# Kernel optimization log

Measured on AMD Instinct MI355X. Metric: run time of the kernel, lower is better.

## Reference

```python
import jax, jax.numpy as jnp
import numpy as np

B, T, NH, EX, VOCAB, NLAYER = 8, 510, 12, 768, 256, 6
NBLK = 2 * NLAYER - 1          # 11 blocks, all with out=ex
NE = T + 2                     # CustomEmb output dim = n_embd = 512
HD = EX // NH
EXIT_SCALE = 1.0 / float(np.sqrt(4 * NBLK))  # torch init divides 'exit' params by sqrt(#exit params)


def _ln(x, s, b):
    m = jnp.mean(x, axis=-1, keepdims=True)
    v = jnp.mean((x - m) ** 2, axis=-1, keepdims=True)
    return (x - m) * jax.lax.rsqrt(v + 1e-5) * s + b


def setup_inputs() -> dict:
    key = jax.random.key(0)
    ks = iter(jax.random.split(key, 40))
    def n(shape, scale=0.02):
        return jax.random.normal(next(ks), shape, jnp.float32) * scale
    inp = {}
    inp['idx'] = jax.random.randint(next(ks), (B, T), 0, 2)
    inp['lin_w'] = n((NE, EX)); inp['lin_b'] = n((EX,))
    # stacked per-block params (leading dim NBLK), torch Linear math y = x @ W + b with W stored (in,out)
    inp['ln1_s'] = jnp.ones((NBLK, EX), jnp.float32); inp['ln1_b'] = jnp.zeros((NBLK, EX), jnp.float32)
    inp['qw'] = n((NBLK, EX, EX)); inp['qb'] = n((NBLK, EX))
    inp['kw'] = n((NBLK, EX, EX)); inp['kb'] = n((NBLK, EX))
    inp['vw'] = n((NBLK, EX, EX)); inp['vb'] = n((NBLK, EX))
    inp['ew'] = n((NBLK, EX, EX)) * EXIT_SCALE; inp['eb'] = n((NBLK, EX)) * EXIT_SCALE
    inp['ln2_s'] = jnp.ones((NBLK, EX), jnp.float32); inp['ln2_b'] = jnp.zeros((NBLK, EX), jnp.float32)
    inp['m1w'] = n((NBLK, EX, 4 * EX)); inp['m1b'] = n((NBLK, 4 * EX))
    inp['m2w'] = n((NBLK, 4 * EX, EX)) * EXIT_SCALE; inp['m2b'] = n((NBLK, EX)) * EXIT_SCALE
    inp['lnf_s'] = jnp.ones((EX,), jnp.float32); inp['lnf_b'] = jnp.zeros((EX,), jnp.float32)
    inp['head_w'] = n((EX * T, VOCAB)); inp['head_b'] = n((VOCAB,))
    return inp


def reference(idx, lin_w, lin_b, ln1_s, ln1_b, qw, qb, kw, kb, vw, vb, ew, eb,
              ln2_s, ln2_b, m1w, m1b, m2w, m2b, lnf_s, lnf_b, head_w, head_b):
    # CustomEmb: one-hot of binary token + identity positional encoding -> [B,T,T+2]
    e0 = (idx == 0).astype(jnp.float32)
    e1 = (idx == 1).astype(jnp.float32)
    pos = jnp.broadcast_to(jnp.eye(T, dtype=jnp.float32), (B, T, T))
    x = jnp.concatenate([e0[:, :, None], e1[:, :, None], pos], axis=2)
    x = jax.nn.relu(x @ lin_w + lin_b)                       # [B,T,EX]
    mask = jnp.tril(jnp.ones((T, T), bool))
    inv_sqrt_d = 1.0 / float(np.sqrt(HD))

    def block(x, p):
        l1s, l1b, Qw, Qb, Kw, Kb, Vw, Vb, Ew, Eb, l2s, l2b, M1w, M1b, M2w, M2b = p
        h = _ln(x, l1s, l1b)
        q = (h @ Qw + Qb).reshape(B, T, NH, HD)
        k = (h @ Kw + Kb).reshape(B, T, NH, HD)
        v = (h @ Vw + Vb).reshape(B, T, NH, HD)
        att = jnp.einsum('bqhd,bkhd->bhqk', q, k) * inv_sqrt_d
        att = jnp.where(mask, att, -jnp.inf)
        probs = jax.nn.softmax(att, axis=-1)
        y = jnp.einsum('bhqk,bkhd->bqhd', probs, v).reshape(B, T, EX)
        x = x + y @ Ew + Eb
        h2 = _ln(x, l2s, l2b)
        x = x + jax.nn.relu(h2 @ M1w + M1b) @ M2w + M2b      # MLP depth=2: initial+relu+exit
        return x, None

    x, _ = jax.lax.scan(block, x, (ln1_s, ln1_b, qw, qb, kw, kb, vw, vb,
                                   ew, eb, ln2_s, ln2_b, m1w, m1b, m2w, m2b))
    x = _ln(x, lnf_s, lnf_b)
    return x.reshape(B, -1) @ head_w + head_b                # [B, VOCAB]
```

## Files before the change

### kernel.cpp

```cpp
#include <hip/hip_runtime.h>
#include <hip/hip_bf16.h>
#include <math.h>

constexpr int cB = 8, cT = 510, cNH = 12, cEX = 768, cVOC = 256, cNBLK = 11, cHD = 64;
constexpr int cMB = 512;
constexpr int cMP = 4096;
constexpr int cQKV = 3 * cEX;

typedef __attribute__((ext_vector_type(8))) short bf16x8;
typedef __attribute__((ext_vector_type(4))) float f32x4;
using bf16 = __hip_bfloat16;

__device__ inline void gload16(const void* g, void* l) {
    __builtin_amdgcn_global_load_lds((const __attribute__((address_space(1))) unsigned int*)g,
                                     (__attribute__((address_space(3))) unsigned int*)l, 16, 0, 0);
}
__device__ inline short f2bs(float f) {
    bf16 b = __float2bfloat16(f);
    return *reinterpret_cast<short*>(&b);
}
__device__ inline float bs2f(unsigned short s) {
    unsigned int u = ((unsigned int)s) << 16;
    float f;
    __builtin_memcpy(&f, &u, 4);
    return f;
}

__global__ __launch_bounds__(256) void embed_kernel(
    const int* __restrict__ idx, const float* __restrict__ lin_w,
    const float* __restrict__ lin_b, short* __restrict__ x)
{
    int row = blockIdx.x;
    int b = row >> 9, t = row & 511;
    short* xr = x + (size_t)row * cEX;
    if (t >= cT) {
        for (int j = threadIdx.x; j < cEX; j += 256) xr[j] = 0;
        return;
    }
    int tok = idx[b * cT + t] & 1;
    const float* wt = lin_w + (size_t)tok * cEX;
    const float* wp = lin_w + (size_t)(2 + t) * cEX;
    for (int j = threadIdx.x; j < cEX; j += 256) {
        float val = wt[j] + wp[j] + lin_b[j];
        xr[j] = f2bs(fmaxf(val, 0.0f));
    }
}

__global__ __launch_bounds__(256) void ln_wave(
    const short* __restrict__ in, const float* __restrict__ s,
    const float* __restrict__ bsh, short* __restrict__ out)
{
    const int wid = threadIdx.x >> 6, lane = threadIdx.x & 63;
    const int row = blockIdx.x * 4 + wid;
    const short* xr = in + (size_t)row * cEX;
    float v[12];
    float sum = 0.f, sq = 0.f;
#pragma unroll
    for (int p = 0; p < 3; ++p) {
        ushort4 raw = *(const ushort4*)&xr[p * 256 + lane * 4];
        v[p * 4 + 0] = bs2f(raw.x); v[p * 4 + 1] = bs2f(raw.y);
        v[p * 4 + 2] = bs2f(raw.z); v[p * 4 + 3] = bs2f(raw.w);
#pragma unroll
        for (int q = 0; q < 4; ++q) { sum += v[p * 4 + q]; sq += v[p * 4 + q] * v[p * 4 + q]; }
    }
#pragma unroll
    for (int off = 1; off < 64; off <<= 1) {
        sum += __shfl_xor(sum, off, 64);
        sq  += __shfl_xor(sq, off, 64);
    }
    float mean = sum * (1.0f / cEX);
    float var = sq * (1.0f / cEX) - mean * mean;
    float rstd = rsqrtf(var + 1e-5f);
    short* outr = out + (size_t)row * cEX;
#pragma unroll
    for (int p = 0; p < 3; ++p) {
        int c = p * 256 + lane * 4;
        float4 sv = *(const float4*)&s[c];
        float4 bv = *(const float4*)&bsh[c];
        short4 pk;
        pk.x = f2bs((v[p * 4 + 0] - mean) * rstd * sv.x + bv.x);
        pk.y = f2bs((v[p * 4 + 1] - mean) * rstd * sv.y + bv.y);
        pk.z = f2bs((v[p * 4 + 2] - mean) * rstd * sv.z + bv.z);
        pk.w = f2bs((v[p * 4 + 3] - mean) * rstd * sv.w + bv.w);
        *(short4*)&outr[c] = pk;
    }
}

__global__ __launch_bounds__(256) void transpose_w(
    const float* __restrict__ W, bf16* __restrict__ WT,
    int K, int N, size_t w_stride, size_t wt_stride, int wt_row_off)
{
    __shared__ float t[32][33];
    const float* Wb = W + (size_t)blockIdx.z * w_stride;
    bf16* WTb = WT + (size_t)blockIdx.z * wt_stride;
    int n0 = blockIdx.x * 32, k0 = blockIdx.y * 32;
    int c = threadIdx.x & 31, ty = threadIdx.x >> 5;
#pragma unroll
    for (int it = 0; it < 4; ++it) {
        int r = ty + it * 8;
        t[r][c] = Wb[(size_t)(k0 + r) * N + n0 + c];
    }
    __syncthreads();
#pragma unroll
    for (int it = 0; it < 4; ++it) {
        int a = ty + it * 8;
        WTb[(size_t)(wt_row_off + n0 + a) * K + k0 + c] = __float2bfloat16(t[c][a]);
    }
}

__global__ __launch_bounds__(256) void transpose_qkv(
    const float* __restrict__ qw, const float* __restrict__ kw,
    const float* __restrict__ vw, bf16* __restrict__ WT)
{
    __shared__ float t[32][33];
    int z = blockIdx.z;
    int blk = z / 3, which = z - blk * 3;
    const float* Wb = (which == 0 ? qw : which == 1 ? kw : vw) + (size_t)blk * cEX * cEX;
    bf16* WTb = WT + (size_t)blk * cQKV * cEX + (size_t)which * cEX * cEX;
    int n0 = blockIdx.x * 32, k0 = blockIdx.y * 32;
    int c = threadIdx.x & 31, ty = threadIdx.x >> 5;
#pragma unroll
    for (int it = 0; it < 4; ++it) {
        int r = ty + it * 8;
        t[r][c] = Wb[(size_t)(k0 + r) * cEX + n0 + c];
    }
    __syncthreads();
#pragma unroll
    for (int it = 0; it < 4; ++it) {
        int a = ty + it * 8;
        WTb[(size_t)(n0 + a) * cEX + k0 + c] = __float2bfloat16(t[c][a]);
    }
}

__global__ __launch_bounds__(256) void concat_bias(
    const float* __restrict__ qb, const float* __restrict__ kb,
    const float* __restrict__ vb, float* __restrict__ qkvb)
{
    int i = blockIdx.x * 256 + threadIdx.x;
    if (i >= cNBLK * cQKV) return;
    int blk = i / cQKV, c = i - blk * cQKV;
    const float* src; int cc = c;
    if (c < cEX)            { src = qb; }
    else if (c < 2 * cEX)   { src = kb; cc = c - cEX; }
    else                    { src = vb; cc = c - 2 * cEX; }
    qkvb[i] = src[(size_t)blk * cEX + cc];
}

template<int FM, int FN, bool RELU, bool RESID, bool OUTBF16, bool VT>
__global__ __launch_bounds__(256) void gemm_db(
    const short* __restrict__ A, const short* __restrict__ BT,
    const float* __restrict__ bias, const short* __restrict__ resid,
    void* __restrict__ Cout, short* __restrict__ vTr, int K, int N)
{
    constexpr int BM = FM * 32, BN = FN * 32;
    constexpr int TS = (BM + BN) * 64;
    constexpr int CA = BM / 32, CB = BN / 32;
    constexpr int LPT = CA + CB;
    static_assert(LPT >= 5 && LPT <= 8, "vmcnt literal range");
    __shared__ short lds[2 * TS];
    const int tid = threadIdx.x;
    const int lane = tid & 63, wid = tid >> 6;
    const int wm = wid >> 1, wn = wid & 1;
    const int bm = blockIdx.y * BM, bn = blockIdx.x * BN;
    const int li = lane & 15, gk = lane >> 4;

    f32x4 acc[FM][FN];
#pragma unroll
    for (int i = 0; i < FM; ++i)
#pragma unroll
        for (int j = 0; j < FN; ++j)
            acc[i][j] = f32x4{0.f, 0.f, 0.f, 0.f};

    auto stage = [&](int kt, int buf) {
        short* la = &lds[buf * TS];
        short* lb = la + BM * 64;
#pragma unroll
        for (int i = 0; i < CA; ++i) {
            int s = i * 256 + tid;
            int r = s >> 3, c = s & 7;
            gload16(A + (size_t)(bm + r) * K + kt * 64 + (c ^ (r & 7)) * 8,
                    (char*)la + (size_t)(i * 256 + wid * 64) * 16);
        }
#pragma unroll
        for (int i = 0; i < CB; ++i) {
            int s = i * 256 + tid;
            int r = s >> 3, c = s & 7;
            gload16(BT + (size_t)(bn + r) * K + kt * 64 + (c ^ (r & 7)) * 8,
                    (char*)lb + (size_t)(i * 256 + wid * 64) * 16);
        }
    };

    const int nkt = K >> 6;
    stage(0, 0);
    stage(1, 1);

    for (int t = 0; t < nkt; ++t) {
        if (t + 1 < nkt) {
            if constexpr (LPT == 5)      asm volatile("s_waitcnt vmcnt(5)" ::: "memory");
            else if constexpr (LPT == 6) asm volatile("s_waitcnt vmcnt(6)" ::: "memory");
            else if constexpr (LPT == 7) asm volatile("s_waitcnt vmcnt(7)" ::: "memory");
            else                         asm volatile("s_waitcnt vmcnt(8)" ::: "memory");
        } else {
            asm volatile("s_waitcnt vmcnt(0)" ::: "memory");
        }
        __builtin_amdgcn_s_barrier();

        const short* la = &lds[(t & 1) * TS];
        const short* lb = la + BM * 64;

        bf16x8 af0[FM], bf0[FN];
#pragma unroll
        for (int mi = 0; mi < FM; ++mi) {
            int row = (wm * FM + mi) * 16 + li;
            af0[mi] = *(const bf16x8*)&la[row * 64 + (gk ^ (row & 7)) * 8];
        }
#pragma unroll
        for (int ni = 0; ni < FN; ++ni) {
            int row = (wn * FN + ni) * 16 + li;
            bf0[ni] = *(const bf16x8*)&lb[row * 64 + (gk ^ (row & 7)) * 8];
        }
        __builtin_amdgcn_s_setprio(1);
#pragma unroll
        for (int mi = 0; mi < FM; ++mi)
#pragma unroll
            for (int ni = 0; ni < FN; ++ni)
                acc[mi][ni] = __builtin_amdgcn_mfma_f32_16x16x32_bf16(
                    af0[mi], bf0[ni], acc[mi][ni], 0, 0, 0);
        __builtin_amdgcn_s_setprio(0);

        bf16x8 af1[FM], bf1[FN];
#pragma unroll
        for (int mi = 0; mi < FM; ++mi) {
            int row = (wm * FM + mi) * 16 + li;
            af1[mi] = *(const bf16x8*)&la[row * 64 + ((4 + gk) ^ (row & 7)) * 8];
        }
#pragma unroll
        for (int ni = 0; ni < FN; ++ni) {
            int row = (wn * FN + ni) * 16 + li;
            bf1[ni] = *(const bf16x8*)&lb[row * 64 + ((4 + gk) ^ (row & 7)) * 8];
        }
        asm volatile("s_waitcnt lgkmcnt(0)" ::: "memory");
        __builtin_amdgcn_s_barrier();
        if (t + 2 < nkt) stage(t + 2, t & 1);
        __builtin_amdgcn_s_setprio(1);
#pragma unroll
        for (int mi = 0; mi < FM; ++mi)
#pragma unroll
            for (int ni = 0; ni < FN; ++ni)
                acc[mi][ni] = __builtin_amdgcn_mfma_f32_16x16x32_bf16(
                    af1[mi], bf1[ni], acc[mi][ni], 0, 0, 0);
        __builtin_amdgcn_s_setprio(0);
    }

#pragma unroll
    for (int mi = 0; mi < FM; ++mi) {
#pragma unroll
        for (int ni = 0; ni < FN; ++ni) {
            int col = bn + (wn * FN + ni) * 16 + li;
            float bv = bias[col];
            int row0 = bm + (wm * FM + mi) * 16 + gk * 4;
            if (VT && col >= 2 * cEX) {
                short4 pk;
                pk.x = f2bs(acc[mi][ni][0] + bv);
                pk.y = f2bs(acc[mi][ni][1] + bv);
                pk.z = f2bs(acc[mi][ni][2] + bv);
                pk.w = f2bs(acc[mi][ni][3] + bv);
                *(short4*)&vTr[(size_t)(col - 2 * cEX) * cMP + row0] = pk;
            } else {
#pragma unroll
                for (int j = 0; j < 4; ++j) {
                    int row = row0 + j;
                    float v = acc[mi][ni][j] + bv;
                    if (RELU) v = fmaxf(v, 0.0f);
                    if (RESID) v += bs2f((unsigned short)resid[(size_t)row * N + col]);
                    if (OUTBF16)
                        ((bf16*)Cout)[(size_t)row * N + col] = __float2bfloat16(v);
                    else
                        ((float*)Cout)[(size_t)row * N + col] = v;
                }
            }
        }
    }
}

__global__ __launch_bounds__(256) void attn_mfma(
    const short* __restrict__ qkv, const short* __restrict__ vT, bf16* __restrict__ y)
{
    const int qt = blockIdx.x, h = blockIdx.y, b = blockIdx.z;
    __shared__ short Ks[2][64 * 64];
    __shared__ short Vs[2][64 * 64];
    __shared__ short Ss[4][16][72];
    const int tid = threadIdx.x;
    const int lane = tid & 63, wid = tid >> 6;
    const int li = lane & 15, gk = lane >> 4;

    const size_t rowb = (size_t)b * cMB;
    int qr = qt * 64 + wid * 16 + li;
    int qrc = qr < cT ? qr : cT - 1;
    const short* qrow = qkv + (rowb + qrc) * cQKV + h * cHD;
    bf16x8 qf0 = *(const bf16x8*)(qrow + gk * 8);
    bf16x8 qf1 = *(const bf16x8*)(qrow + 32 + gk * 8);

    f32x4 o[4];
    float mrow[4], lrow[4];
#pragma unroll
    for (int dt = 0; dt < 4; ++dt) o[dt] = f32x4{0.f, 0.f, 0.f, 0.f};
#pragma unroll
    for (int j = 0; j < 4; ++j) { mrow[j] = -3e38f; lrow[j] = 0.f; }

    const int qloc = qt * 64 + wid * 16 + gk * 4;

    auto stage = [&](int kt, int buf) {
#pragma unroll
        for (int i = 0; i < 2; ++i) {
            int s = i * 256 + tid;
            int r = s >> 3, c = s & 7;
            gload16(qkv + (rowb + kt * 64 + r) * cQKV + cEX + h * cHD + (c ^ (r & 7)) * 8,
                    (char*)&Ks[buf][0] + (size_t)(i * 256 + wid * 64) * 16);
        }
#pragma unroll
        for (int i = 0; i < 2; ++i) {
            int s = i * 256 + tid;
            int d = s >> 3, c = s & 7;
            gload16(vT + (size_t)(h * cHD + d) * cMP + rowb + kt * 64 + (c ^ (d & 7)) * 8,
                    (char*)&Vs[buf][0] + (size_t)(i * 256 + wid * 64) * 16);
        }
    };

    const int nkt = qt + 1;
    stage(0, 0);
    for (int kt = 0; kt < nkt; ++kt) {
        if (kt + 1 < nkt) {
            stage(kt + 1, (kt + 1) & 1);
            asm volatile("s_waitcnt vmcnt(4)" ::: "memory");
        } else {
            asm volatile("s_waitcnt vmcnt(0)" ::: "memory");
        }
        __builtin_amdgcn_s_barrier();
        const int cur = kt & 1;

        f32x4 sg[4];
#pragma unroll
        for (int g = 0; g < 4; ++g) sg[g] = f32x4{0.f, 0.f, 0.f, 0.f};
#pragma unroll
        for (int g = 0; g < 4; ++g) {
            int key = g * 16 + li;
            bf16x8 k0 = *(const bf16x8*)&Ks[cur][key * 64 + (gk ^ (key & 7)) * 8];
            bf16x8 k1 = *(const bf16x8*)&Ks[cur][key * 64 + ((4 + gk) ^ (key & 7)) * 8];
            sg[g] = __builtin_amdgcn_mfma_f32_16x16x32_bf16(qf0, k0, sg[g], 0, 0, 0);
            sg[g] = __builtin_amdgcn_mfma_f32_16x16x32_bf16(qf1, k1, sg[g], 0, 0, 0);
        }

#pragma unroll
        for (int j = 0; j < 4; ++j) {
            int q = qloc + j;
            float sc[4];
#pragma unroll
            for (int g = 0; g < 4; ++g) {
                int kg = kt * 64 + g * 16 + li;
                sc[g] = (kg <= q) ? sg[g][j] * 0.125f : -3e38f;
            }
            float tm = fmaxf(fmaxf(sc[0], sc[1]), fmaxf(sc[2], sc[3]));
            tm = fmaxf(tm, __shfl_xor(tm, 1, 16));
            tm = fmaxf(tm, __shfl_xor(tm, 2, 16));
            tm = fmaxf(tm, __shfl_xor(tm, 4, 16));
            tm = fmaxf(tm, __shfl_xor(tm, 8, 16));
            float mnew = fmaxf(mrow[j], tm);
            float p[4], ps = 0.f;
#pragma unroll
            for (int g = 0; g < 4; ++g) { p[g] = __expf(sc[g] - mnew); ps += p[g]; }
            ps += __shfl_xor(ps, 1, 16);
            ps += __shfl_xor(ps, 2, 16);
            ps += __shfl_xor(ps, 4, 16);
            ps += __shfl_xor(ps, 8, 16);
            float scale = __expf(mrow[j] - mnew);
            lrow[j] = lrow[j] * scale + ps;
            mrow[j] = mnew;
#pragma unroll
            for (int dt = 0; dt < 4; ++dt) o[dt][j] *= scale;
#pragma unroll
            for (int g = 0; g < 4; ++g)
                Ss[wid][gk * 4 + j][g * 16 + li] = f2bs(p[g]);
        }

        bf16x8 pa0 = *(const bf16x8*)&Ss[wid][li][gk * 8];
        bf16x8 pa1 = *(const bf16x8*)&Ss[wid][li][32 + gk * 8];
#pragma unroll
        for (int dt = 0; dt < 4; ++dt) {
            int d = dt * 16 + li;
            bf16x8 vf0 = *(const bf16x8*)&Vs[cur][d * 64 + (gk ^ (d & 7)) * 8];
            bf16x8 vf1 = *(const bf16x8*)&Vs[cur][d * 64 + ((4 + gk) ^ (d & 7)) * 8];
            o[dt] = __builtin_amdgcn_mfma_f32_16x16x32_bf16(pa0, vf0, o[dt], 0, 0, 0);
            o[dt] = __builtin_amdgcn_mfma_f32_16x16x32_bf16(pa1, vf1, o[dt], 0, 0, 0);
        }
        asm volatile("s_waitcnt lgkmcnt(0)" ::: "memory");
        __builtin_amdgcn_s_barrier();
    }

#pragma unroll
    for (int j = 0; j < 4; ++j) {
        int q = qloc + j;
        if (q >= cT) continue;
        float inv = 1.0f / lrow[j];
        bf16* yr = y + (rowb + q) * cEX + h * cHD;
#pragma unroll
        for (int dt = 0; dt < 4; ++dt)
            yr[dt * 16 + li] = __float2bfloat16(o[dt][j] * inv);
    }
}

__global__ __launch_bounds__(256) void head_part_kernel(
    const short* __restrict__ x, const float* __restrict__ lnf_s,
    const float* __restrict__ lnf_b, const float* __restrict__ hw,
    float* __restrict__ part)
{
    __shared__ float xs[8][1536];
    __shared__ float stat[16][2];
    const int tid = threadIdx.x;
    const int trow0 = blockIdx.x * 2;
    const int wid = tid >> 6, lane = tid & 63;
    {
        const int g = lane >> 4, li = lane & 15;
        const int p = wid * 4 + g, bb = p >> 1, rr = p & 1;
        const short* xr = x + ((size_t)(bb * cMB + trow0 + rr)) * cEX;
        float sum = 0.f, sq = 0.f;
#pragma unroll
        for (int it = 0; it < 12; ++it) {
            ushort4 raw = *(const ushort4*)&xr[it * 64 + li * 4];
            float a0 = bs2f(raw.x), a1 = bs2f(raw.y), a2 = bs2f(raw.z), a3 = bs2f(raw.w);
            sum += a0 + a1 + a2 + a3;
            sq  += a0 * a0 + a1 * a1 + a2 * a2 + a3 * a3;
        }
#pragma unroll
        for (int off = 8; off > 0; off >>= 1) {
            sum += __shfl_xor(sum, off, 16);
            sq  += __shfl_xor(sq, off, 16);
        }
        if (li == 0) {
            float mean = sum * (1.0f / cEX);
            float var = sq * (1.0f / cEX) - mean * mean;
            stat[p][0] = mean;
            stat[p][1] = rsqrtf(var + 1e-5f);
        }
    }
    __syncthreads();
    for (int i = tid; i < 8 * 1536; i += 256) {
        int bb = i / 1536, kk = i - bb * 1536;
        int rr = kk >= cEX ? 1 : 0;
        int e = kk - rr * cEX;
        float mean = stat[bb * 2 + rr][0], rstd = stat[bb * 2 + rr][1];
        float val = bs2f((unsigned short)x[((size_t)(bb * cMB + trow0 + rr)) * cEX + e]);
        xs[bb][kk] = (val - mean) * rstd * lnf_s[e] + lnf_b[e];
    }
    __syncthreads();
    float acc[8] = {};
    const int k0 = blockIdx.x * 1536;
    const float* wp = hw + (size_t)k0 * cVOC + tid;
    for (int kk = 0; kk < 1536; ++kk) {
        float w = wp[(size_t)kk * cVOC];
#pragma unroll
        for (int bb = 0; bb < 8; ++bb) acc[bb] += xs[bb][kk] * w;
    }
#pragma unroll
    for (int bb = 0; bb < 8; ++bb)
        part[((size_t)blockIdx.x * 8 + bb) * cVOC + tid] = acc[bb];
}

__global__ __launch_bounds__(256) void head_reduce_kernel(
    const float* __restrict__ part, const float* __restrict__ hb, float* __restrict__ out)
{
    int i = blockIdx.x * 256 + threadIdx.x;
    int bb = i >> 8, vv = i & 255;
    float acc = hb[vv];
    for (int c = 0; c < 255; ++c) acc += part[((size_t)c * 8 + bb) * 256 + vv];
    out[i] = acc;
}

extern "C" void kernel_launch(void* const* d_in, const int* in_sizes, int n_in,
                              void* d_out, int out_size, void* d_ws, size_t ws_size,
                              hipStream_t stream) {
    (void)in_sizes; (void)n_in; (void)out_size; (void)ws_size;
    const int*   idx    = (const int*)d_in[0];
    const float* lin_w  = (const float*)d_in[1];
    const float* lin_b  = (const float*)d_in[2];
    const float* ln1_s  = (const float*)d_in[3];
    const float* ln1_b  = (const float*)d_in[4];
    const float* qw     = (const float*)d_in[5];
    const float* qbias  = (const float*)d_in[6];
    const float* kw     = (const float*)d_in[7];
    const float* kbias  = (const float*)d_in[8];
    const float* vw     = (const float*)d_in[9];
    const float* vbias  = (const float*)d_in[10];
    const float* ew     = (const float*)d_in[11];
    const float* ebias  = (const float*)d_in[12];
    const float* ln2_s  = (const float*)d_in[13];
    const float* ln2_b  = (const float*)d_in[14];
    const float* m1w    = (const float*)d_in[15];
    const float* m1b    = (const float*)d_in[16];
    const float* m2w    = (const float*)d_in[17];
    const float* m2b    = (const float*)d_in[18];
    const float* lnf_s  = (const float*)d_in[19];
    const float* lnf_b  = (const float*)d_in[20];
    const float* head_w = (const float*)d_in[21];
    const float* head_b = (const float*)d_in[22];
    float* out = (float*)d_out;

    const size_t act = (size_t)cMP * cEX;
    float* part = (float*)d_ws;
    float* qkvb = part + 255 * 8 * 256;
    short* x    = (short*)(qkvb + cNBLK * cQKV);
    short* qkv  = x + act;
    short* vTr  = qkv + (size_t)cMP * cQKV;
    short* h    = vTr + (size_t)cEX * cMP;
    short* h2   = h + act;
    short* y    = h2 + act;
    short* u    = y + act;
    short* wqkvT = u + (size_t)cMP * 4 * cEX;
    short* weT   = wqkvT + (size_t)cNBLK * cQKV * cEX;
    short* wm1T  = weT + (size_t)cNBLK * cEX * cEX;
    short* wm2T  = wm1T + (size_t)cNBLK * cEX * 4 * cEX;

    transpose_qkv<<<dim3(24, 24, 3 * cNBLK), 256, 0, stream>>>(qw, kw, vw, (bf16*)wqkvT);
    transpose_w<<<dim3(24, 24, cNBLK), 256, 0, stream>>>(ew, (bf16*)weT, cEX, cEX,
        (size_t)cEX * cEX, (size_t)cEX * cEX, 0);
    transpose_w<<<dim3(96, 24, cNBLK), 256, 0, stream>>>(m1w, (bf16*)wm1T, cEX, 4 * cEX,
        (size_t)cEX * 4 * cEX, (size_t)cEX * 4 * cEX, 0);
    transpose_w<<<dim3(24, 96, cNBLK), 256, 0, stream>>>(m2w, (bf16*)wm2T, 4 * cEX, cEX,
        (size_t)cEX * 4 * cEX, (size_t)cEX * 4 * cEX, 0);
    concat_bias<<<(cNBLK * cQKV + 255) / 256, 256, 0, stream>>>(qbias, kbias, vbias, qkvb);

    embed_kernel<<<cMP, 256, 0, stream>>>(idx, lin_w, lin_b, x);

    for (int blk = 0; blk < cNBLK; ++blk) {
        size_t bo = (size_t)blk * cEX;
        ln_wave<<<cMP / 4, 256, 0, stream>>>(x, ln1_s + bo, ln1_b + bo, h);
        gemm_db<4, 3, false, false, true, true><<<dim3(cQKV / 96, cMP / 128), 256, 0, stream>>>(
            h, wqkvT + (size_t)blk * cQKV * cEX, qkvb + (size_t)blk * cQKV, nullptr,
            qkv, vTr, cEX, cQKV);
        attn_mfma<<<dim3(8, cNH, cB), 256, 0, stream>>>(qkv, vTr, (bf16*)y);
        gemm_db<2, 3, false, true, true, false><<<dim3(cEX / 96, cMP / 64), 256, 0, stream>>>(
            y, weT + (size_t)blk * cEX * cEX, ebias + bo, x, x, nullptr, cEX, cEX);
        ln_wave<<<cMP / 4, 256, 0, stream>>>(x, ln2_s + bo, ln2_b + bo, h2);
        gemm_db<4, 4, true, false, true, false><<<dim3(4 * cEX / 128, cMP / 128), 256, 0, stream>>>(
            h2, wm1T + (size_t)blk * cEX * 4 * cEX, m1b + (size_t)blk * 4 * cEX, nullptr,
            u, nullptr, cEX, 4 * cEX);
        gemm_db<2, 3, false, true, true, false><<<dim3(cEX / 96, cMP / 64), 256, 0, stream>>>(
            u, wm2T + (size_t)blk * cEX * 4 * cEX, m2b + bo, x, x, nullptr, 4 * cEX, cEX);
    }
    head_part_kernel<<<255, 256, 0, stream>>>(x, lnf_s, lnf_b, head_w, part);
    head_reduce_kernel<<<8, 256, 0, stream>>>(part, head_b, out);
}
```

Before: 1.718 ms.

## Use 32x32x16 MFMA GEMM with 128x128 tiles for QKV and MLP-up projections

Adds a new GEMM kernel built on 32x32x16 bf16 MFMA instructions with 128x128 block tiles, double-buffered LDS and an XOR-swizzled layout. The QKV projection (which also writes V transposed) and the first MLP projection now use it. The larger MFMA shape cuts LDS fragment loads per FLOP and raises arithmetic intensity. In exchange, the QKV grid changes from 96-wide to 128-wide tiles, and the epilogue stores are strided scalar bf16 writes, which may coalesce poorly.

```diff
diff --git a/kernel.cpp b/kernel.cpp
--- a/kernel.cpp
+++ b/kernel.cpp
@@ -9,6 +9,7 @@
 
 typedef __attribute__((ext_vector_type(8))) short bf16x8;
 typedef __attribute__((ext_vector_type(4))) float f32x4;
+typedef __attribute__((ext_vector_type(16))) float f32x16;
 using bf16 = __hip_bfloat16;
 
 __device__ inline void gload16(const void* g, void* l) {
@@ -146,11 +147,154 @@
     qkvb[i] = src[(size_t)blk * cEX + cc];
 }
 
-template<int FM, int FN, bool RELU, bool RESID, bool OUTBF16, bool VT>
+template<bool RELU, bool VT>
+__global__ __launch_bounds__(256) void gemm32(
+    const short* __restrict__ A, const short* __restrict__ BT,
+    const float* __restrict__ bias, void* __restrict__ Cout,
+    short* __restrict__ vTr, int K, int N)
+{
+    constexpr int BM = 128, BN = 128;
+    constexpr int TS = (BM + BN) * 64;
+    __shared__ short lds[2 * TS];
+    const int tid = threadIdx.x;
+    const int lane = tid & 63, wid = tid >> 6;
+    const int wm = wid >> 1, wn = wid & 1;
+    const int bm = blockIdx.y * BM, bn = blockIdx.x * BN;
+    const int l32 = lane & 31, kh = lane >> 5;
+
+    f32x16 acc[2][2];
+#pragma unroll
+    for (int i = 0; i < 2; ++i)
+#pragma unroll
+        for (int j = 0; j < 2; ++j)
+            acc[i][j] = f32x16{0.f,0.f,0.f,0.f,0.f,0.f,0.f,0.f,
+                               0.f,0.f,0.f,0.f,0.f,0.f,0.f,0.f};
+
+    auto stage = [&](int kt, int buf) {
+        short* la = &lds[buf * TS];
+        short* lb = la + BM * 64;
+#pragma unroll
+        for (int i = 0; i < 4; ++i) {
+            int s = i * 256 + tid;
+            int r = s >> 3, c = s & 7;
+            gload16(A + (size_t)(bm + r) * K + kt * 64 + (c ^ (r & 7)) * 8,
+                    (char*)la + (size_t)(i * 256 + wid * 64) * 16);
+        }
+#pragma unroll
+        for (int i = 0; i < 4; ++i) {
+            int s = i * 256 + tid;
+            int r = s >> 3, c = s & 7;
+            gload16(BT + (size_t)(bn + r) * K + kt * 64 + (c ^ (r & 7)) * 8,
+                    (char*)lb + (size_t)(i * 256 + wid * 64) * 16);
+        }
+    };
+
+    const int nkt = K >> 6;
+    stage(0, 0);
+    stage(1, 1);
+
+    for (int t = 0; t < nkt; ++t) {
+        if (t + 1 < nkt) asm volatile("s_waitcnt vmcnt(8)" ::: "memory");
+        else             asm volatile("s_waitcnt vmcnt(0)" ::: "memory");
+        __builtin_amdgcn_s_barrier();
+
+        const short* la = &lds[(t & 1) * TS];
+        const short* lb = la + BM * 64;
+
+        bf16x8 af0[2][2], bf0[2][2];
+#pragma unroll
+        for (int mi = 0; mi < 2; ++mi) {
+            int row = (wm * 2 + mi) * 32 + l32;
+#pragma unroll
+            for (int ks = 0; ks < 2; ++ks)
+                af0[mi][ks] = *(const bf16x8*)&la[row * 64 + ((ks * 2 + kh) ^ (row & 7)) * 8];
+        }
+#pragma unroll
+        for (int ni = 0; ni < 2; ++ni) {
+            int row = (wn * 2 + ni) * 32 + l32;
+#pragma unroll
+            for (int ks = 0; ks < 2; ++ks)
+                bf0[ni][ks] = *(const bf16x8*)&lb[row * 64 + ((ks * 2 + kh) ^ (row & 7)) * 8];
+        }
+        __builtin_amdgcn_s_setprio(1);
+#pragma unroll
+        for (int ks = 0; ks < 2; ++ks)
+#pragma unroll
+            for (int mi = 0; mi < 2; ++mi)
+#pragma unroll
+                for (int ni = 0; ni < 2; ++ni)
+                    acc[mi][ni] = __builtin_amdgcn_mfma_f32_32x32x16_bf16(
+                        af0[mi][ks], bf0[ni][ks], acc[mi][ni], 0, 0, 0);
+        __builtin_amdgcn_s_setprio(0);
+
+        bf16x8 af1[2][2], bf1[2][2];
+#pragma unroll
+        for (int mi = 0; mi < 2; ++mi) {
+            int row = (wm * 2 + mi) * 32 + l32;
+#pragma unroll
+            for (int ks = 0; ks < 2; ++ks)
+                af1[mi][ks] = *(const bf16x8*)&la[row * 64 + (((ks + 2) * 2 + kh) ^ (row & 7)) * 8];
+        }
+#pragma unroll
+        for (int ni = 0; ni < 2; ++ni) {
+            int row = (wn * 2 + ni) * 32 + l32;
+#pragma unroll
+            for (int ks = 0; ks < 2; ++ks)
+                bf1[ni][ks] = *(const bf16x8*)&lb[row * 64 + (((ks + 2) * 2 + kh) ^ (row & 7)) * 8];
+        }
+        asm volatile("s_waitcnt lgkmcnt(0)" ::: "memory");
+        __builtin_amdgcn_s_barrier();
+        if (t + 2 < nkt) stage(t + 2, t & 1);
+        __builtin_amdgcn_s_setprio(1);
+#pragma unroll
+        for (int ks = 0; ks < 2; ++ks)
+#pragma unroll
+            for (int mi = 0; mi < 2; ++mi)
+#pragma unroll
+                for (int ni = 0; ni < 2; ++ni)
+                    acc[mi][ni] = __builtin_amdgcn_mfma_f32_32x32x16_bf16(
+                        af1[mi][ks], bf1[ni][ks], acc[mi][ni], 0, 0, 0);
+        __builtin_amdgcn_s_setprio(0);
+    }
+
+#pragma unroll
+    for (int mi = 0; mi < 2; ++mi) {
+#pragma unroll
+        for (int ni = 0; ni < 2; ++ni) {
+            int col = bn + (wn * 2 + ni) * 32 + l32;
+            float bv = bias[col];
+            int rbase = bm + (wm * 2 + mi) * 32 + 4 * kh;
+            if (VT && col >= 2 * cEX) {
+#pragma unroll
+                for (int g = 0; g < 4; ++g) {
+                    int r0 = rbase + 8 * g;
+                    short4 pk;
+                    pk.x = f2bs(acc[mi][ni][g * 4 + 0] + bv);
+                    pk.y = f2bs(acc[mi][ni][g * 4 + 1] + bv);
+                    pk.z = f2bs(acc[mi][ni][g * 4 + 2] + bv);
+                    pk.w = f2bs(acc[mi][ni][g * 4 + 3] + bv);
+                    *(short4*)&vTr[(size_t)(col - 2 * cEX) * cMP + r0] = pk;
+                }
+            } else {
+#pragma unroll
+                for (int g = 0; g < 4; ++g)
+#pragma unroll
+                    for (int j = 0; j < 4; ++j) {
+                        int row = rbase + 8 * g + j;
+                        float v = acc[mi][ni][g * 4 + j] + bv;
+                        if (RELU) v = fmaxf(v, 0.0f);
+                        ((bf16*)Cout)[(size_t)row * N + col] = __float2bfloat16(v);
+                    }
+            }
+        }
+    }
+}
+
+template<int FM, int FN, bool RELU, bool RESID, bool OUTBF16>
 __global__ __launch_bounds__(256) void gemm_db(
     const short* __restrict__ A, const short* __restrict__ BT,
     const float* __restrict__ bias, const short* __restrict__ resid,
-    void* __restrict__ Cout, short* __restrict__ vTr, int K, int N)
+    void* __restrict__ Cout, int K, int N)
 {
     constexpr int BM = FM * 32, BN = FN * 32;
     constexpr int TS = (BM + BN) * 64;
@@ -259,25 +403,16 @@
             int col = bn + (wn * FN + ni) * 16 + li;
             float bv = bias[col];
             int row0 = bm + (wm * FM + mi) * 16 + gk * 4;
-            if (VT && col >= 2 * cEX) {
-                short4 pk;
-                pk.x = f2bs(acc[mi][ni][0] + bv);
-                pk.y = f2bs(acc[mi][ni][1] + bv);
-                pk.z = f2bs(acc[mi][ni][2] + bv);
-                pk.w = f2bs(acc[mi][ni][3] + bv);
-                *(short4*)&vTr[(size_t)(col - 2 * cEX) * cMP + row0] = pk;
-            } else {
-#pragma unroll
-                for (int j = 0; j < 4; ++j) {
-                    int row = row0 + j;
-                    float v = acc[mi][ni][j] + bv;
-                    if (RELU) v = fmaxf(v, 0.0f);
-                    if (RESID) v += bs2f((unsigned short)resid[(size_t)row * N + col]);
-                    if (OUTBF16)
-                        ((bf16*)Cout)[(size_t)row * N + col] = __float2bfloat16(v);
-                    else
-                        ((float*)Cout)[(size_t)row * N + col] = v;
-                }
+#pragma unroll
+            for (int j = 0; j < 4; ++j) {
+                int row = row0 + j;
+                float v = acc[mi][ni][j] + bv;
+                if (RELU) v = fmaxf(v, 0.0f);
+                if (RESID) v += bs2f((unsigned short)resid[(size_t)row * N + col]);
+                if (OUTBF16)
+                    ((bf16*)Cout)[(size_t)row * N + col] = __float2bfloat16(v);
+                else
+                    ((float*)Cout)[(size_t)row * N + col] = v;
             }
         }
     }
@@ -534,18 +669,18 @@
     for (int blk = 0; blk < cNBLK; ++blk) {
         size_t bo = (size_t)blk * cEX;
         ln_wave<<<cMP / 4, 256, 0, stream>>>(x, ln1_s + bo, ln1_b + bo, h);
-        gemm_db<4, 3, false, false, true, true><<<dim3(cQKV / 96, cMP / 128), 256, 0, stream>>>(
-            h, wqkvT + (size_t)blk * cQKV * cEX, qkvb + (size_t)blk * cQKV, nullptr,
+        gemm32<false, true><<<dim3(cQKV / 128, cMP / 128), 256, 0, stream>>>(
+            h, wqkvT + (size_t)blk * cQKV * cEX, qkvb + (size_t)blk * cQKV,
             qkv, vTr, cEX, cQKV);
         attn_mfma<<<dim3(8, cNH, cB), 256, 0, stream>>>(qkv, vTr, (bf16*)y);
-        gemm_db<2, 3, false, true, true, false><<<dim3(cEX / 96, cMP / 64), 256, 0, stream>>>(
-            y, weT + (size_t)blk * cEX * cEX, ebias + bo, x, x, nullptr, cEX, cEX);
+        gemm_db<2, 3, false, true, true><<<dim3(cEX / 96, cMP / 64), 256, 0, stream>>>(
+            y, weT + (size_t)blk * cEX * cEX, ebias + bo, x, x, cEX, cEX);
         ln_wave<<<cMP / 4, 256, 0, stream>>>(x, ln2_s + bo, ln2_b + bo, h2);
-        gemm_db<4, 4, true, false, true, false><<<dim3(4 * cEX / 128, cMP / 128), 256, 0, stream>>>(
-            h2, wm1T + (size_t)blk * cEX * 4 * cEX, m1b + (size_t)blk * 4 * cEX, nullptr,
+        gemm32<true, false><<<dim3(4 * cEX / 128, cMP / 128), 256, 0, stream>>>(
+            h2, wm1T + (size_t)blk * cEX * 4 * cEX, m1b + (size_t)blk * 4 * cEX,
             u, nullptr, cEX, 4 * cEX);
-        gemm_db<2, 3, false, true, true, false><<<dim3(cEX / 96, cMP / 64), 256, 0, stream>>>(
-            u, wm2T + (size_t)blk * cEX * 4 * cEX, m2b + bo, x, x, nullptr, 4 * cEX, cEX);
+        gemm_db<2, 3, false, true, true><<<dim3(cEX / 96, cMP / 64), 256, 0, stream>>>(
+            u, wm2T + (size_t)blk * cEX * 4 * cEX, m2b + bo, x, x, 4 * cEX, cEX);
     }
     head_part_kernel<<<255, 256, 0, stream>>>(x, lnf_s, lnf_b, head_w, part);
     head_reduce_kernel<<<8, 256, 0, stream>>>(part, head_b, out);
```

Result: slower. 1.801 ms (+4.8%).
